# Optimization experiments

Measured on AMD Instinct MI355X. Metric: run time of the kernel, lower is better.

Reference implementation:

```python
import jax, jax.numpy as jnp
import numpy as np

N = 50000        # nodes
E = 800000       # random edges (self loops appended inside reference, per PyG default)
IN = 128         # in_channels
H1, C1 = 8, 64   # conv1: heads, hidden_channels
NUM_CLASSES = 2  # conv2 out (heads=1, concat=False)
NEG_SLOPE = 0.2  # PyG GATConv default LeakyReLU slope


def setup_inputs() -> dict:
    key = jax.random.key(0)
    ks = jax.random.split(key, 12)
    x = jax.random.normal(ks[0], (N, IN), dtype=jnp.float32)
    edge_index = jax.random.randint(ks[1], (2, E), 0, N)
    # conv1 params: W1 [IN, H1*C1], att vectors [H1, C1], bias [H1*C1]
    W1 = jax.random.normal(ks[2], (IN, H1 * C1), dtype=jnp.float32) / np.sqrt(IN)
    a_src1 = jax.random.normal(ks[3], (H1, C1), dtype=jnp.float32) / np.sqrt(C1)
    a_dst1 = jax.random.normal(ks[4], (H1, C1), dtype=jnp.float32) / np.sqrt(C1)
    b1 = jnp.zeros((H1 * C1,), dtype=jnp.float32)
    # conv2 params: heads=1, out=NUM_CLASSES
    W2 = jax.random.normal(ks[5], (H1 * C1, 1 * NUM_CLASSES), dtype=jnp.float32) / np.sqrt(H1 * C1)
    a_src2 = jax.random.normal(ks[6], (1, NUM_CLASSES), dtype=jnp.float32) / np.sqrt(NUM_CLASSES)
    a_dst2 = jax.random.normal(ks[7], (1, NUM_CLASSES), dtype=jnp.float32) / np.sqrt(NUM_CLASSES)
    b2 = jnp.zeros((NUM_CLASSES,), dtype=jnp.float32)
    return {"x": x, "edge_index": edge_index, "W1": W1, "a_src1": a_src1,
            "a_dst1": a_dst1, "b1": b1, "W2": W2, "a_src2": a_src2,
            "a_dst2": a_dst2, "b2": b2}


def gat_layer(x, src, dst, W, a_src, a_dst, bias, concat):
    n = x.shape[0]
    heads, ch = a_src.shape
    h = (x @ W).reshape(n, heads, ch)                      # [N,H,C]
    alpha_s = jnp.einsum('nhc,hc->nh', h, a_src)           # per-node src score
    alpha_d = jnp.einsum('nhc,hc->nh', h, a_dst)           # per-node dst score
    e = jax.nn.leaky_relu(alpha_s[src] + alpha_d[dst], NEG_SLOPE)  # [Etot,H]
    # segment softmax over edges grouped by destination node
    m = jax.ops.segment_max(e, dst, num_segments=n)
    ex = jnp.exp(e - m[dst])
    den = jax.ops.segment_sum(ex, dst, num_segments=n)
    alpha = ex / den[dst]                                  # [Etot,H]
    out = jax.ops.segment_sum(h[src] * alpha[:, :, None], dst, num_segments=n)  # [N,H,C]
    out = out.reshape(n, heads * ch) if concat else out.mean(axis=1)
    return out + bias


def reference(x, edge_index, W1, a_src1, a_dst1, b1, W2, a_src2, a_dst2, b2):
    n = x.shape[0]
    loops = jnp.arange(n, dtype=edge_index.dtype)
    src = jnp.concatenate([edge_index[0], loops])   # PyG add_self_loops=True
    dst = jnp.concatenate([edge_index[1], loops])
    h = gat_layer(x, src, dst, W1, a_src1, a_dst1, b1, concat=True)   # [N, H1*C1]
    h = jax.nn.elu(h)
    # dropout is identity in eval mode
    out = gat_layer(h, src, dst, W2, a_src2, a_dst2, b2, concat=False)  # [N, 2]
    return out
```

## Files before the change

kernel.cpp:

```cpp
#include <hip/hip_runtime.h>
#include <hip/hip_bf16.h>

#define NEG 0.2f
#define BKT 64

typedef __attribute__((ext_vector_type(8))) short bf16x8;
typedef __attribute__((ext_vector_type(4))) float f32x4;

static __device__ __forceinline__ unsigned short f2bf(float f) {
    union { float f; unsigned u; } v; v.f = f;
    unsigned r = v.u + 0x7fff + ((v.u >> 16) & 1);
    return (unsigned short)(r >> 16);
}
static __device__ __forceinline__ float bf_lo(unsigned u) {
    return __uint_as_float(u << 16);
}
static __device__ __forceinline__ float bf_hi(unsigned u) {
    return __uint_as_float(u & 0xffff0000u);
}

__global__ void k_init(int* __restrict__ deg, unsigned short* __restrict__ csr, int n) {
    int v = blockIdx.x * 256 + threadIdx.x;
    if (v >= n) return;
    deg[v] = 1;
    csr[(size_t)v * BKT] = (unsigned short)v;
}

__global__ __launch_bounds__(256) void k_big(const int* __restrict__ ei,
                                             int* __restrict__ deg,
                                             unsigned short* __restrict__ csr,
                                             const float* __restrict__ x,
                                             const float* __restrict__ W1,
                                             const float* __restrict__ a_src,
                                             const float* __restrict__ a_dst,
                                             unsigned short* __restrict__ h1b,
                                             float* __restrict__ as1,
                                             float* __restrict__ ad1,
                                             int E_, int n, int gblocks) {
    int tid = threadIdx.x;
    if ((int)blockIdx.x >= gblocks) {
        int e = (blockIdx.x - gblocks) * 256 + tid;
        if (e >= E_) return;
        int s = ei[e], d = ei[E_ + e];
        int slot = atomicAdd(&deg[d], 1);
        if (slot < BKT) csr[(size_t)d * BKT + slot] = (unsigned short)s;
        return;
    }
    __shared__ unsigned short stg[4][16][72];
    int g = blockIdx.x;
    int j = g & 7, rb = g >> 3;
    int wave = tid >> 6, lane = tid & 63;
    int l15 = lane & 15, q = lane >> 4;
    int col0 = j * 64;
    int rowblk = rb * 256 + wave * 64;

    bf16x8 bfr[4][4];
    #pragma unroll
    for (int kb = 0; kb < 4; kb++)
        #pragma unroll
        for (int t = 0; t < 4; t++) {
            const float* wp = W1 + (size_t)(kb * 32 + q * 8) * 512 + col0 + t * 16 + l15;
            #pragma unroll
            for (int e = 0; e < 8; e++)
                bfr[kb][t][e] = (short)f2bf(wp[(size_t)e * 512]);
        }
    float asv[4], adv[4];
    #pragma unroll
    for (int t = 0; t < 4; t++) {
        asv[t] = a_src[j * 64 + t * 16 + l15];
        adv[t] = a_dst[j * 64 + t * 16 + l15];
    }

    #pragma unroll
    for (int st = 0; st < 4; st++) {
        int row0 = rowblk + st * 16;
        int ar = row0 + l15; if (ar > n - 1) ar = n - 1;
        f32x4 acc[4] = {};
        const float* ap = x + (size_t)ar * 128 + q * 8;
        #pragma unroll
        for (int kb = 0; kb < 4; kb++) {
            float4 v0 = *(const float4*)(ap + kb * 32);
            float4 v1 = *(const float4*)(ap + kb * 32 + 4);
            bf16x8 af;
            af[0] = (short)f2bf(v0.x); af[1] = (short)f2bf(v0.y);
            af[2] = (short)f2bf(v0.z); af[3] = (short)f2bf(v0.w);
            af[4] = (short)f2bf(v1.x); af[5] = (short)f2bf(v1.y);
            af[6] = (short)f2bf(v1.z); af[7] = (short)f2bf(v1.w);
            #pragma unroll
            for (int t = 0; t < 4; t++)
                acc[t] = __builtin_amdgcn_mfma_f32_16x16x32_bf16(af, bfr[kb][t], acc[t], 0, 0, 0);
        }
        #pragma unroll
        for (int t = 0; t < 4; t++)
            #pragma unroll
            for (int r = 0; r < 4; r++)
                stg[wave][q * 4 + r][t * 16 + l15] = f2bf(acc[t][r]);
        #pragma unroll
        for (int p = 0; p < 2; p++) {
            int lr = p * 8 + (lane >> 3);
            int row = row0 + lr;
            int cd = (lane & 7) * 8;
            uint4 vv = *(const uint4*)&stg[wave][lr][cd];
            if (row < n)
                *(uint4*)(h1b + (size_t)row * 512 + col0 + cd) = vv;
        }
        float ps[4], pd[4];
        #pragma unroll
        for (int r = 0; r < 4; r++) {
            ps[r] = acc[0][r] * asv[0] + acc[1][r] * asv[1]
                  + acc[2][r] * asv[2] + acc[3][r] * asv[3];
            pd[r] = acc[0][r] * adv[0] + acc[1][r] * adv[1]
                  + acc[2][r] * adv[2] + acc[3][r] * adv[3];
            #pragma unroll
            for (int off = 1; off < 16; off <<= 1) {
                ps[r] += __shfl_xor(ps[r], off, 64);
                pd[r] += __shfl_xor(pd[r], off, 64);
            }
        }
        if (l15 < 4) {
            int r = l15;
            float vps = ps[0], vpd = pd[0];
            if (r == 1) { vps = ps[1]; vpd = pd[1]; }
            if (r == 2) { vps = ps[2]; vpd = pd[2]; }
            if (r == 3) { vps = ps[3]; vpd = pd[3]; }
            int row = row0 + q * 4 + r;
            if (row < n) { as1[row * 8 + j] = vps; ad1[row * 8 + j] = vpd; }
        }
    }
}

__global__ __launch_bounds__(256) void k_agg1(const unsigned short* __restrict__ h1b,
                                              const float* __restrict__ as1,
                                              const float* __restrict__ ad1,
                                              const float* __restrict__ b1,
                                              const float* __restrict__ W2,
                                              const int* __restrict__ deg,
                                              const unsigned short* __restrict__ csr,
                                              float* __restrict__ h2, int n) {
    int lane = threadIdx.x & 63;
    int v = blockIdx.x * 4 + (threadIdx.x >> 6);
    if (v >= n) return;
    int head = lane >> 3, c = lane * 8;
    int dv = deg[v]; if (dv > BKT) dv = BKT;
    const unsigned short* cp = csr + (size_t)v * BKT;
    float adh = ad1[v * 8 + head];
    float s = 0.f;
    float acc[8] = {};
    int i = 0;
    for (; i + 4 <= dv; i += 4) {
        ushort4 uu = *(const ushort4*)(cp + i);
        int u0 = uu.x, u1 = uu.y, u2 = uu.z, u3 = uu.w;
        float ea = as1[u0 * 8 + head] + adh;
        float eb = as1[u1 * 8 + head] + adh;
        float ec = as1[u2 * 8 + head] + adh;
        float ed = as1[u3 * 8 + head] + adh;
        uint4 h0 = *(const uint4*)(h1b + (size_t)u0 * 512 + c);
        uint4 h1 = *(const uint4*)(h1b + (size_t)u1 * 512 + c);
        uint4 h2v = *(const uint4*)(h1b + (size_t)u2 * 512 + c);
        uint4 h3 = *(const uint4*)(h1b + (size_t)u3 * 512 + c);
        ea = (ea >= 0.f) ? ea : NEG * ea;
        eb = (eb >= 0.f) ? eb : NEG * eb;
        ec = (ec >= 0.f) ? ec : NEG * ec;
        ed = (ed >= 0.f) ? ed : NEG * ed;
        float w0 = __expf(ea), w1 = __expf(eb), w2 = __expf(ec), w3 = __expf(ed);
        s += (w0 + w1) + (w2 + w3);
        acc[0] = fmaf(w3, bf_lo(h3.x), fmaf(w2, bf_lo(h2v.x), fmaf(w1, bf_lo(h1.x), fmaf(w0, bf_lo(h0.x), acc[0]))));
        acc[1] = fmaf(w3, bf_hi(h3.x), fmaf(w2, bf_hi(h2v.x), fmaf(w1, bf_hi(h1.x), fmaf(w0, bf_hi(h0.x), acc[1]))));
        acc[2] = fmaf(w3, bf_lo(h3.y), fmaf(w2, bf_lo(h2v.y), fmaf(w1, bf_lo(h1.y), fmaf(w0, bf_lo(h0.y), acc[2]))));
        acc[3] = fmaf(w3, bf_hi(h3.y), fmaf(w2, bf_hi(h2v.y), fmaf(w1, bf_hi(h1.y), fmaf(w0, bf_hi(h0.y), acc[3]))));
        acc[4] = fmaf(w3, bf_lo(h3.z), fmaf(w2, bf_lo(h2v.z), fmaf(w1, bf_lo(h1.z), fmaf(w0, bf_lo(h0.z), acc[4]))));
        acc[5] = fmaf(w3, bf_hi(h3.z), fmaf(w2, bf_hi(h2v.z), fmaf(w1, bf_hi(h1.z), fmaf(w0, bf_hi(h0.z), acc[5]))));
        acc[6] = fmaf(w3, bf_lo(h3.w), fmaf(w2, bf_lo(h2v.w), fmaf(w1, bf_lo(h1.w), fmaf(w0, bf_lo(h0.w), acc[6]))));
        acc[7] = fmaf(w3, bf_hi(h3.w), fmaf(w2, bf_hi(h2v.w), fmaf(w1, bf_hi(h1.w), fmaf(w0, bf_hi(h0.w), acc[7]))));
    }
    for (; i < dv; i++) {
        int u = cp[i];
        float e = as1[u * 8 + head] + adh;
        e = (e >= 0.f) ? e : NEG * e;
        float w = __expf(e);
        s += w;
        uint4 hv = *(const uint4*)(h1b + (size_t)u * 512 + c);
        acc[0] = fmaf(w, bf_lo(hv.x), acc[0]);
        acc[1] = fmaf(w, bf_hi(hv.x), acc[1]);
        acc[2] = fmaf(w, bf_lo(hv.y), acc[2]);
        acc[3] = fmaf(w, bf_hi(hv.y), acc[3]);
        acc[4] = fmaf(w, bf_lo(hv.z), acc[4]);
        acc[5] = fmaf(w, bf_hi(hv.z), acc[5]);
        acc[6] = fmaf(w, bf_lo(hv.w), acc[6]);
        acc[7] = fmaf(w, bf_hi(hv.w), acc[7]);
    }
    float inv = 1.0f / s;
    float4 ba = *(const float4*)(b1 + c);
    float4 bb = *(const float4*)(b1 + c + 4);
    float o[8] = {acc[0] * inv + ba.x, acc[1] * inv + ba.y,
                  acc[2] * inv + ba.z, acc[3] * inv + ba.w,
                  acc[4] * inv + bb.x, acc[5] * inv + bb.y,
                  acc[6] * inv + bb.z, acc[7] * inv + bb.w};
    #pragma unroll
    for (int jj = 0; jj < 8; jj++)
        o[jj] = (o[jj] > 0.f) ? o[jj] : (__expf(o[jj]) - 1.0f);
    const float4* wp = (const float4*)(W2 + c * 2);
    float4 w0 = wp[0], w1 = wp[1], w2 = wp[2], w3 = wp[3];
    float p0 = o[0] * w0.x + o[1] * w0.z + o[2] * w1.x + o[3] * w1.z
             + o[4] * w2.x + o[5] * w2.z + o[6] * w3.x + o[7] * w3.z;
    float p1 = o[0] * w0.y + o[1] * w0.w + o[2] * w1.y + o[3] * w1.w
             + o[4] * w2.y + o[5] * w2.w + o[6] * w3.y + o[7] * w3.w;
    #pragma unroll
    for (int off = 1; off < 64; off <<= 1) {
        p0 += __shfl_xor(p0, off, 64);
        p1 += __shfl_xor(p1, off, 64);
    }
    if (lane == 0) {
        h2[2 * v] = p0;
        h2[2 * v + 1] = p1;
    }
}

__global__ __launch_bounds__(256) void k_agg2(const float* __restrict__ h2,
                                              const float* __restrict__ a_src2,
                                              const float* __restrict__ a_dst2,
                                              const float* __restrict__ b2,
                                              const int* __restrict__ deg,
                                              const unsigned short* __restrict__ csr,
                                              float* __restrict__ out, int n) {
    int tid = threadIdx.x;
    int lane = tid & 63, wave = tid >> 6;
    int sub = lane & 7, g = lane >> 3;
    int v = blockIdx.x * 32 + wave * 8 + g;
    if (v >= n) return;
    int dv = deg[v]; if (dv > BKT) dv = BKT;
    const unsigned short* cp = csr + (size_t)v * BKT;
    float sa0 = a_src2[0], sa1 = a_src2[1];
    float da0 = a_dst2[0], da1 = a_dst2[1];
    float2 hv = *(const float2*)(h2 + 2 * v);
    float adv = hv.x * da0 + hv.y * da1;
    float s = 0.f, a0 = 0.f, a1 = 0.f;
    for (int i = sub; i < dv; i += 8) {
        int u = cp[i];
        float2 hu = *(const float2*)(h2 + 2 * u);
        float e = hu.x * sa0 + hu.y * sa1 + adv;
        e = (e >= 0.f) ? e : NEG * e;
        float w = __expf(e);
        s += w;
        a0 = fmaf(w, hu.x, a0);
        a1 = fmaf(w, hu.y, a1);
    }
    #pragma unroll
    for (int off = 1; off < 8; off <<= 1) {
        s  += __shfl_xor(s, off, 64);
        a0 += __shfl_xor(a0, off, 64);
        a1 += __shfl_xor(a1, off, 64);
    }
    if (sub == 0) {
        float inv = 1.0f / s;
        out[2 * v]     = a0 * inv + b2[0];
        out[2 * v + 1] = a1 * inv + b2[1];
    }
}

extern "C" void kernel_launch(void* const* d_in, const int* in_sizes, int n_in,
                              void* d_out, int out_size, void* d_ws, size_t ws_size,
                              hipStream_t stream) {
    const float* x      = (const float*)d_in[0];
    const int*   ei     = (const int*)d_in[1];
    const float* W1     = (const float*)d_in[2];
    const float* a_src1 = (const float*)d_in[3];
    const float* a_dst1 = (const float*)d_in[4];
    const float* b1     = (const float*)d_in[5];
    const float* W2     = (const float*)d_in[6];
    const float* a_src2 = (const float*)d_in[7];
    const float* a_dst2 = (const float*)d_in[8];
    const float* b2     = (const float*)d_in[9];
    float* out = (float*)d_out;

    int n  = in_sizes[0] / 128;
    int E_ = in_sizes[1] / 2;
    int rblk = (n + 255) / 256;
    int npad = rblk * 256;

    char* w = (char*)d_ws;
    auto alloc = [&](size_t bytes) {
        char* p = w; w += (bytes + 255) & ~(size_t)255; return p;
    };
    int*            deg    = (int*)alloc((size_t)n * 4);
    unsigned short* csr    = (unsigned short*)alloc((size_t)n * BKT * 2);
    unsigned short* h1b    = (unsigned short*)alloc((size_t)npad * 512 * 2);
    float*          as1    = (float*)alloc((size_t)n * 8 * 4);
    float*          ad1    = (float*)alloc((size_t)n * 8 * 4);
    float*          h2     = (float*)alloc((size_t)n * 2 * 4);

    int nb256 = (n + 255) / 256;
    k_init<<<nb256, 256, 0, stream>>>(deg, csr, n);

    int gblocks = rblk * 8;
    int sblocks = (E_ + 255) / 256;
    k_big<<<gblocks + sblocks, 256, 0, stream>>>(ei, deg, csr, x, W1,
                                                 a_src1, a_dst1, h1b, as1, ad1,
                                                 E_, n, gblocks);

    int nb = (n + 3) / 4;
    k_agg1<<<nb, 256, 0, stream>>>(h1b, as1, ad1, b1, W2, deg, csr, h2, n);

    int ab = (n + 31) / 32;
    k_agg2<<<ab, 256, 0, stream>>>(h2, a_src2, a_dst2, b2, deg, csr, out, n);
}
```

Before: 308.0 us.

## Store layer-1 features head-major and aggregate per head with atomic reduction

The layer-1 bf16 features and attention scores move from node-major to head-major slices, so each head's 64 channels for all nodes are contiguous. Aggregation is split so each block handles one head for 16 nodes, with 16 lanes per node. Partial conv2 projections from each head are accumulated into h2 with float atomics, and h2 is zeroed in the init kernel. The goal is a per-head working set (about 6.4MB per slice) that fits in L2/MALL for the random gathers, at the cost of 8x more csr and degree reads and extra atomics.

```diff
diff --git a/kernel.cpp b/kernel.cpp
--- a/kernel.cpp
+++ b/kernel.cpp
@@ -12,18 +12,18 @@
     unsigned r = v.u + 0x7fff + ((v.u >> 16) & 1);
     return (unsigned short)(r >> 16);
 }
-static __device__ __forceinline__ float bf_lo(unsigned u) {
-    return __uint_as_float(u << 16);
-}
-static __device__ __forceinline__ float bf_hi(unsigned u) {
-    return __uint_as_float(u & 0xffff0000u);
-}
-
-__global__ void k_init(int* __restrict__ deg, unsigned short* __restrict__ csr, int n) {
+static __device__ __forceinline__ float bfs(unsigned short h) {
+    return __uint_as_float((unsigned)h << 16);
+}
+
+__global__ void k_init(int* __restrict__ deg, unsigned short* __restrict__ csr,
+                       float* __restrict__ h2, int n) {
     int v = blockIdx.x * 256 + threadIdx.x;
     if (v >= n) return;
     deg[v] = 1;
     csr[(size_t)v * BKT] = (unsigned short)v;
+    h2[2 * v] = 0.f;
+    h2[2 * v + 1] = 0.f;
 }
 
 __global__ __launch_bounds__(256) void k_big(const int* __restrict__ ei,
@@ -33,10 +33,10 @@
                                              const float* __restrict__ W1,
                                              const float* __restrict__ a_src,
                                              const float* __restrict__ a_dst,
-                                             unsigned short* __restrict__ h1b,
-                                             float* __restrict__ as1,
-                                             float* __restrict__ ad1,
-                                             int E_, int n, int gblocks) {
+                                             unsigned short* __restrict__ h1s,
+                                             float* __restrict__ as1t,
+                                             float* __restrict__ ad1t,
+                                             int E_, int n, int npad, int gblocks) {
     int tid = threadIdx.x;
     if ((int)blockIdx.x >= gblocks) {
         int e = (blockIdx.x - gblocks) * 256 + tid;
@@ -53,6 +53,7 @@
     int l15 = lane & 15, q = lane >> 4;
     int col0 = j * 64;
     int rowblk = rb * 256 + wave * 64;
+    unsigned short* hslice = h1s + (size_t)j * npad * 64;
 
     bf16x8 bfr[4][4];
     #pragma unroll
@@ -102,7 +103,7 @@
             int cd = (lane & 7) * 8;
             uint4 vv = *(const uint4*)&stg[wave][lr][cd];
             if (row < n)
-                *(uint4*)(h1b + (size_t)row * 512 + col0 + cd) = vv;
+                *(uint4*)(hslice + (size_t)row * 64 + cd) = vv;
         }
         float ps[4], pd[4];
         #pragma unroll
@@ -124,95 +125,86 @@
             if (r == 2) { vps = ps[2]; vpd = pd[2]; }
             if (r == 3) { vps = ps[3]; vpd = pd[3]; }
             int row = row0 + q * 4 + r;
-            if (row < n) { as1[row * 8 + j] = vps; ad1[row * 8 + j] = vpd; }
-        }
-    }
-}
-
-__global__ __launch_bounds__(256) void k_agg1(const unsigned short* __restrict__ h1b,
-                                              const float* __restrict__ as1,
-                                              const float* __restrict__ ad1,
-                                              const float* __restrict__ b1,
-                                              const float* __restrict__ W2,
-                                              const int* __restrict__ deg,
-                                              const unsigned short* __restrict__ csr,
-                                              float* __restrict__ h2, int n) {
-    int lane = threadIdx.x & 63;
-    int v = blockIdx.x * 4 + (threadIdx.x >> 6);
-    if (v >= n) return;
-    int head = lane >> 3, c = lane * 8;
-    int dv = deg[v]; if (dv > BKT) dv = BKT;
-    const unsigned short* cp = csr + (size_t)v * BKT;
-    float adh = ad1[v * 8 + head];
-    float s = 0.f;
-    float acc[8] = {};
+            if (row < n) {
+                as1t[(size_t)j * n + row] = vps;
+                ad1t[(size_t)j * n + row] = vpd;
+            }
+        }
+    }
+}
+
+__global__ __launch_bounds__(256) void k_agg1h(const unsigned short* __restrict__ h1s,
+                                               const float* __restrict__ as1t,
+                                               const float* __restrict__ ad1t,
+                                               const float* __restrict__ b1,
+                                               const float* __restrict__ W2,
+                                               const int* __restrict__ deg,
+                                               const unsigned short* __restrict__ csr,
+                                               float* __restrict__ h2, int n, int npad) {
+    int tid = threadIdx.x;
+    int head = blockIdx.x & 7, grp = blockIdx.x >> 3;
+    int wave = tid >> 6, lane = tid & 63;
+    int sub = lane >> 4, li = lane & 15;
+    int v = grp * 16 + wave * 4 + sub;
+    bool act = (v < n);
+    int vc = act ? v : (n - 1);
+    int dv = act ? deg[vc] : 0; if (dv > BKT) dv = BKT;
+    const unsigned short* cp = csr + (size_t)vc * BKT;
+    const float* as_h = as1t + (size_t)head * n;
+    float adh = ad1t[(size_t)head * n + vc];
+    const unsigned short* hs = h1s + (size_t)head * npad * 64 + li * 4;
+    float s = 0.f, a0 = 0.f, a1 = 0.f, a2 = 0.f, a3 = 0.f;
     int i = 0;
-    for (; i + 4 <= dv; i += 4) {
-        ushort4 uu = *(const ushort4*)(cp + i);
-        int u0 = uu.x, u1 = uu.y, u2 = uu.z, u3 = uu.w;
-        float ea = as1[u0 * 8 + head] + adh;
-        float eb = as1[u1 * 8 + head] + adh;
-        float ec = as1[u2 * 8 + head] + adh;
-        float ed = as1[u3 * 8 + head] + adh;
-        uint4 h0 = *(const uint4*)(h1b + (size_t)u0 * 512 + c);
-        uint4 h1 = *(const uint4*)(h1b + (size_t)u1 * 512 + c);
-        uint4 h2v = *(const uint4*)(h1b + (size_t)u2 * 512 + c);
-        uint4 h3 = *(const uint4*)(h1b + (size_t)u3 * 512 + c);
-        ea = (ea >= 0.f) ? ea : NEG * ea;
-        eb = (eb >= 0.f) ? eb : NEG * eb;
-        ec = (ec >= 0.f) ? ec : NEG * ec;
-        ed = (ed >= 0.f) ? ed : NEG * ed;
-        float w0 = __expf(ea), w1 = __expf(eb), w2 = __expf(ec), w3 = __expf(ed);
-        s += (w0 + w1) + (w2 + w3);
-        acc[0] = fmaf(w3, bf_lo(h3.x), fmaf(w2, bf_lo(h2v.x), fmaf(w1, bf_lo(h1.x), fmaf(w0, bf_lo(h0.x), acc[0]))));
-        acc[1] = fmaf(w3, bf_hi(h3.x), fmaf(w2, bf_hi(h2v.x), fmaf(w1, bf_hi(h1.x), fmaf(w0, bf_hi(h0.x), acc[1]))));
-        acc[2] = fmaf(w3, bf_lo(h3.y), fmaf(w2, bf_lo(h2v.y), fmaf(w1, bf_lo(h1.y), fmaf(w0, bf_lo(h0.y), acc[2]))));
-        acc[3] = fmaf(w3, bf_hi(h3.y), fmaf(w2, bf_hi(h2v.y), fmaf(w1, bf_hi(h1.y), fmaf(w0, bf_hi(h0.y), acc[3]))));
-        acc[4] = fmaf(w3, bf_lo(h3.z), fmaf(w2, bf_lo(h2v.z), fmaf(w1, bf_lo(h1.z), fmaf(w0, bf_lo(h0.z), acc[4]))));
-        acc[5] = fmaf(w3, bf_hi(h3.z), fmaf(w2, bf_hi(h2v.z), fmaf(w1, bf_hi(h1.z), fmaf(w0, bf_hi(h0.z), acc[5]))));
-        acc[6] = fmaf(w3, bf_lo(h3.w), fmaf(w2, bf_lo(h2v.w), fmaf(w1, bf_lo(h1.w), fmaf(w0, bf_lo(h0.w), acc[6]))));
-        acc[7] = fmaf(w3, bf_hi(h3.w), fmaf(w2, bf_hi(h2v.w), fmaf(w1, bf_hi(h1.w), fmaf(w0, bf_hi(h0.w), acc[7]))));
-    }
-    for (; i < dv; i++) {
+    for (; i + 2 <= dv; i += 2) {
+        int u0 = cp[i], u1 = cp[i + 1];
+        float e0 = as_h[u0] + adh;
+        float e1 = as_h[u1] + adh;
+        ushort4 q0 = *(const ushort4*)(hs + (size_t)u0 * 64);
+        ushort4 q1 = *(const ushort4*)(hs + (size_t)u1 * 64);
+        e0 = (e0 >= 0.f) ? e0 : NEG * e0;
+        e1 = (e1 >= 0.f) ? e1 : NEG * e1;
+        float w0 = __expf(e0), w1 = __expf(e1);
+        s += w0 + w1;
+        a0 = fmaf(w1, bfs(q1.x), fmaf(w0, bfs(q0.x), a0));
+        a1 = fmaf(w1, bfs(q1.y), fmaf(w0, bfs(q0.y), a1));
+        a2 = fmaf(w1, bfs(q1.z), fmaf(w0, bfs(q0.z), a2));
+        a3 = fmaf(w1, bfs(q1.w), fmaf(w0, bfs(q0.w), a3));
+    }
+    if (i < dv) {
         int u = cp[i];
-        float e = as1[u * 8 + head] + adh;
+        float e = as_h[u] + adh;
+        ushort4 qv = *(const ushort4*)(hs + (size_t)u * 64);
         e = (e >= 0.f) ? e : NEG * e;
         float w = __expf(e);
         s += w;
-        uint4 hv = *(const uint4*)(h1b + (size_t)u * 512 + c);
-        acc[0] = fmaf(w, bf_lo(hv.x), acc[0]);
-        acc[1] = fmaf(w, bf_hi(hv.x), acc[1]);
-        acc[2] = fmaf(w, bf_lo(hv.y), acc[2]);
-        acc[3] = fmaf(w, bf_hi(hv.y), acc[3]);
-        acc[4] = fmaf(w, bf_lo(hv.z), acc[4]);
-        acc[5] = fmaf(w, bf_hi(hv.z), acc[5]);
-        acc[6] = fmaf(w, bf_lo(hv.w), acc[6]);
-        acc[7] = fmaf(w, bf_hi(hv.w), acc[7]);
-    }
-    float inv = 1.0f / s;
-    float4 ba = *(const float4*)(b1 + c);
-    float4 bb = *(const float4*)(b1 + c + 4);
-    float o[8] = {acc[0] * inv + ba.x, acc[1] * inv + ba.y,
-                  acc[2] * inv + ba.z, acc[3] * inv + ba.w,
-                  acc[4] * inv + bb.x, acc[5] * inv + bb.y,
-                  acc[6] * inv + bb.z, acc[7] * inv + bb.w};
-    #pragma unroll
-    for (int jj = 0; jj < 8; jj++)
-        o[jj] = (o[jj] > 0.f) ? o[jj] : (__expf(o[jj]) - 1.0f);
-    const float4* wp = (const float4*)(W2 + c * 2);
-    float4 w0 = wp[0], w1 = wp[1], w2 = wp[2], w3 = wp[3];
-    float p0 = o[0] * w0.x + o[1] * w0.z + o[2] * w1.x + o[3] * w1.z
-             + o[4] * w2.x + o[5] * w2.z + o[6] * w3.x + o[7] * w3.z;
-    float p1 = o[0] * w0.y + o[1] * w0.w + o[2] * w1.y + o[3] * w1.w
-             + o[4] * w2.y + o[5] * w2.w + o[6] * w3.y + o[7] * w3.w;
-    #pragma unroll
-    for (int off = 1; off < 64; off <<= 1) {
+        a0 = fmaf(w, bfs(qv.x), a0);
+        a1 = fmaf(w, bfs(qv.y), a1);
+        a2 = fmaf(w, bfs(qv.z), a2);
+        a3 = fmaf(w, bfs(qv.w), a3);
+    }
+    float inv = act ? 1.0f / s : 0.f;
+    int c = head * 64 + li * 4;
+    float4 bb = *(const float4*)(b1 + c);
+    float o0 = a0 * inv + bb.x;
+    float o1 = a1 * inv + bb.y;
+    float o2 = a2 * inv + bb.z;
+    float o3 = a3 * inv + bb.w;
+    o0 = (o0 > 0.f) ? o0 : (__expf(o0) - 1.0f);
+    o1 = (o1 > 0.f) ? o1 : (__expf(o1) - 1.0f);
+    o2 = (o2 > 0.f) ? o2 : (__expf(o2) - 1.0f);
+    o3 = (o3 > 0.f) ? o3 : (__expf(o3) - 1.0f);
+    float4 w2a = *(const float4*)(W2 + 2 * c);
+    float4 w2b = *(const float4*)(W2 + 2 * c + 4);
+    float p0 = o0 * w2a.x + o1 * w2a.z + o2 * w2b.x + o3 * w2b.z;
+    float p1 = o0 * w2a.y + o1 * w2a.w + o2 * w2b.y + o3 * w2b.w;
+    #pragma unroll
+    for (int off = 1; off < 16; off <<= 1) {
         p0 += __shfl_xor(p0, off, 64);
         p1 += __shfl_xor(p1, off, 64);
     }
-    if (lane == 0) {
-        h2[2 * v] = p0;
-        h2[2 * v + 1] = p1;
+    if (act && li == 0) {
+        atomicAdd(&h2[2 * v], p0);
+        atomicAdd(&h2[2 * v + 1], p1);
     }
 }
 
@@ -284,22 +276,23 @@
     };
     int*            deg    = (int*)alloc((size_t)n * 4);
     unsigned short* csr    = (unsigned short*)alloc((size_t)n * BKT * 2);
-    unsigned short* h1b    = (unsigned short*)alloc((size_t)npad * 512 * 2);
-    float*          as1    = (float*)alloc((size_t)n * 8 * 4);
-    float*          ad1    = (float*)alloc((size_t)n * 8 * 4);
+    unsigned short* h1s    = (unsigned short*)alloc((size_t)npad * 512 * 2);
+    float*          as1t   = (float*)alloc((size_t)n * 8 * 4);
+    float*          ad1t   = (float*)alloc((size_t)n * 8 * 4);
     float*          h2     = (float*)alloc((size_t)n * 2 * 4);
 
     int nb256 = (n + 255) / 256;
-    k_init<<<nb256, 256, 0, stream>>>(deg, csr, n);
+    k_init<<<nb256, 256, 0, stream>>>(deg, csr, h2, n);
 
     int gblocks = rblk * 8;
     int sblocks = (E_ + 255) / 256;
     k_big<<<gblocks + sblocks, 256, 0, stream>>>(ei, deg, csr, x, W1,
-                                                 a_src1, a_dst1, h1b, as1, ad1,
-                                                 E_, n, gblocks);
-
-    int nb = (n + 3) / 4;
-    k_agg1<<<nb, 256, 0, stream>>>(h1b, as1, ad1, b1, W2, deg, csr, h2, n);
+                                                 a_src1, a_dst1, h1s, as1t, ad1t,
+                                                 E_, n, npad, gblocks);
+
+    int ablocks = ((n + 15) / 16) * 8;
+    k_agg1h<<<ablocks, 256, 0, stream>>>(h1s, as1t, ad1t, b1, W2, deg, csr,
+                                         h2, n, npad);
 
     int ab = (n + 31) / 32;
     k_agg2<<<ab, 256, 0, stream>>>(h2, a_src2, a_dst2, b2, deg, csr, out, n);
```

After: 320.1 us. 1.04x slower.
